# Kernel tuning notes

Measured on AMD Instinct MI355X. Metric: run time of the kernel, lower is better.

## Reference

```python
import jax, jax.numpy as jnp
import numpy as np

D_MODEL = 1024
NHEAD = 16
HEAD_DIM = D_MODEL // NHEAD


def setup_inputs() -> dict:
    key = jax.random.key(0)
    ks = jax.random.split(key, 11)
    B, T = 2, 2048
    s = 1.0 / np.sqrt(D_MODEL)
    return {
        "query": jax.random.normal(ks[0], (B, T, D_MODEL), jnp.float32),
        "key": jax.random.normal(ks[1], (B, T, D_MODEL), jnp.float32),
        "value": jax.random.normal(ks[2], (B, T, D_MODEL), jnp.float32),
        "Wq": jax.random.normal(ks[3], (D_MODEL, D_MODEL), jnp.float32) * s,
        "bq": jnp.zeros((D_MODEL,), jnp.float32),
        "Wk": jax.random.normal(ks[4], (D_MODEL, D_MODEL), jnp.float32) * s,
        "bk": jnp.zeros((D_MODEL,), jnp.float32),
        "Wv": jax.random.normal(ks[5], (D_MODEL, D_MODEL), jnp.float32) * s,
        "bv": jnp.zeros((D_MODEL,), jnp.float32),
        "Wo": jax.random.normal(ks[6], (D_MODEL, D_MODEL), jnp.float32) * s,
        "bo": jnp.zeros((D_MODEL,), jnp.float32),
    }


def reference(query, key, value, Wq, bq, Wk, bk, Wv, bv, Wo, bo):
    B, T, _ = query.shape
    scale = HEAD_DIM ** -0.5
    # Linear projections (torch Linear: x @ W.T + b)
    Q = query @ Wq.T + bq
    K = key @ Wk.T + bk
    V = value @ Wv.T + bv
    # [B, H, T, hd]
    Q = Q.reshape(B, T, NHEAD, HEAD_DIM).transpose(0, 2, 1, 3)
    K = K.reshape(B, T, NHEAD, HEAD_DIM).transpose(0, 2, 1, 3)
    V = V.reshape(B, T, NHEAD, HEAD_DIM).transpose(0, 2, 1, 3)
    # Attention scores [B, H, T, T]
    scores = jnp.einsum("bhqd,bhkd->bhqk", Q, K) * scale
    probs = jax.nn.softmax(scores, axis=-1)
    # dropout is identity in eval mode
    out = jnp.einsum("bhqk,bhkd->bhqd", probs, V)
    out = out.transpose(0, 2, 1, 3).reshape(B, T, D_MODEL)
    return out @ Wo.T + bo
```

## Files before the change

kernel.cpp:

```cpp
#include <hip/hip_runtime.h>
#include <stdint.h>

#define LOG2E_OVER_SQRTHD 0.18033688011112042f
#define SM_BIAS 12.0f

typedef unsigned short u16;
typedef _Float16 f16;
typedef __attribute__((ext_vector_type(4))) float f32x4;
typedef __attribute__((ext_vector_type(16))) float f32x16;
typedef __attribute__((ext_vector_type(8))) _Float16 f16x8;
typedef __attribute__((ext_vector_type(2))) __fp16 fp16x2;
typedef __attribute__((ext_vector_type(2))) unsigned int u32x2v;

static __device__ __forceinline__ u16 f2h_bits(float f) {
  union { f16 h; u16 u; } v; v.h = (f16)f; return v.u;
}
static __device__ __forceinline__ uint32_t pkrtz(float a, float b) {
  union { fp16x2 h; uint32_t u; } v;
  v.h = __builtin_amdgcn_cvt_pkrtz(a, b);
  return v.u;
}

static __device__ __forceinline__ void g2l16(const void* g, void* l) {
  __builtin_amdgcn_global_load_lds((const __attribute__((address_space(1))) void*)g,
                                   (__attribute__((address_space(3))) void*)l,
                                   16, 0, 0);
}

__global__ __launch_bounds__(256) void pack_all(
    const float* __restrict__ q, const float* __restrict__ k, const float* __restrict__ v,
    const float* __restrict__ wq, const float* __restrict__ wk,
    const float* __restrict__ wv, const float* __restrict__ wo,
    u16* __restrict__ X, u16* __restrict__ W) {
  int flat = blockIdx.x * 256 + threadIdx.x;
  const float* src;
  u16* dst;
  int idx;
  if (flat < 3 * 1048576) {
    int z = flat >> 20;
    idx = flat & 1048575;
    src = (z == 0) ? q : (z == 1) ? k : v;
    dst = X + (size_t)z * 4194304;
  } else {
    int f2 = flat - 3 * 1048576;
    int z = f2 >> 18;
    idx = f2 & 262143;
    src = (z == 0) ? wq : (z == 1) ? wk : (z == 2) ? wv : wo;
    dst = W + (size_t)z * 1048576;
  }
  float4 x = ((const float4*)src)[idx];
  ushort4 o;
  o.x = f2h_bits(x.x); o.y = f2h_bits(x.y); o.z = f2h_bits(x.z); o.w = f2h_bits(x.w);
  *(ushort4*)(dst + (size_t)idx * 4) = o;
}

template <bool OUT_F16>
static __device__ __forceinline__ void gemm_body(
    const u16* __restrict__ A, const u16* __restrict__ W,
    const float* __restrict__ bias, void* __restrict__ C,
    int ldc, bool row_bias, float oscale, int bm, int bn) {
  __shared__ u16 As[2][128 * 32];
  __shared__ u16 Bs[2][128 * 32];
  const int tid = threadIdx.x;
  const int lane = tid & 63;
  const int wave = tid >> 6;
  const int wm = wave >> 1, wn = wave & 1;
  const int quad = lane >> 4, l15 = lane & 15;

  f32x4 acc[4][4] = {};

  const int r0 = tid >> 2;
  const int c0 = (tid & 3) * 8;
  const u16* Ab = A + (size_t)bm * 1024 + (size_t)r0 * 1024 + c0;
  const u16* Wb = W + (size_t)bn * 1024 + (size_t)r0 * 1024 + c0;

  g2l16(Ab, As[0] + tid * 8);
  g2l16(Ab + 64 * 1024, As[0] + (256 + tid) * 8);
  g2l16(Wb, Bs[0] + tid * 8);
  g2l16(Wb + 64 * 1024, Bs[0] + (256 + tid) * 8);
  __syncthreads();

  for (int kt = 0; kt < 32; ++kt) {
    const int p = kt & 1;
    if (kt + 1 < 32) {
      const int kc = (kt + 1) * 32;
      g2l16(Ab + kc, As[p ^ 1] + tid * 8);
      g2l16(Ab + 64 * 1024 + kc, As[p ^ 1] + (256 + tid) * 8);
      g2l16(Wb + kc, Bs[p ^ 1] + tid * 8);
      g2l16(Wb + 64 * 1024 + kc, Bs[p ^ 1] + (256 + tid) * 8);
    }
    f16x8 af[4], bw[4];
#pragma unroll
    for (int mt = 0; mt < 4; ++mt)
      af[mt] = *(const f16x8*)(As[p] + (wm * 64 + mt * 16 + l15) * 32 + quad * 8);
#pragma unroll
    for (int nt = 0; nt < 4; ++nt)
      bw[nt] = *(const f16x8*)(Bs[p] + (wn * 64 + nt * 16 + l15) * 32 + quad * 8);
#pragma unroll
    for (int mt = 0; mt < 4; ++mt)
#pragma unroll
      for (int nt = 0; nt < 4; ++nt)
        acc[mt][nt] = __builtin_amdgcn_mfma_f32_16x16x32_f16(af[mt], bw[nt], acc[mt][nt], 0, 0, 0);
    __syncthreads();
  }

#pragma unroll
  for (int mt = 0; mt < 4; ++mt) {
    const int row = bm + wm * 64 + mt * 16 + quad * 4;
#pragma unroll
    for (int nt = 0; nt < 4; ++nt) {
      const int col = bn + wn * 64 + nt * 16 + l15;
      const float bcol = row_bias ? 0.0f : bias[col];
#pragma unroll
      for (int i = 0; i < 4; ++i) {
        const float bb = row_bias ? bias[row + i] : bcol;
        float val = (acc[mt][nt][i] + bb) * oscale;
        if (OUT_F16)
          ((u16*)C)[(size_t)(row + i) * ldc + col] = f2h_bits(val);
        else
          ((float*)C)[(size_t)(row + i) * ldc + col] = val;
      }
    }
  }
}

__global__ __launch_bounds__(256) void gemm_qkv(const u16* __restrict__ X,
    const u16* __restrict__ Wf, const float* __restrict__ bq,
    const float* __restrict__ bk, const float* __restrict__ bv,
    u16* __restrict__ QK, u16* __restrict__ Vt, float qscale) {
  const int i = blockIdx.x;
  const int xcd = i & 7;
  const int jj = i >> 3;
  const int x = jj & 31;
  const int pl = jj >> 5;
  const int pg = xcd + 8 * pl;
  const int y = pg & 7, z = pg >> 3;
  if (z == 0) {
    gemm_body<true>(X, Wf, bq, QK, 1024, false, qscale,
                    x * 128, y * 128);
  } else if (z == 1) {
    gemm_body<true>(X + (size_t)4194304, Wf + (size_t)1048576, bk,
                    QK + (size_t)4194304, 1024, false, 1.0f,
                    x * 128, y * 128);
  } else {
    gemm_body<true>(Wf + (size_t)2 * 1048576, X + (size_t)2 * 4194304, bv,
                    Vt, 4096, true, 1.0f,
                    y * 128, x * 128);
  }
}

__global__ __launch_bounds__(256) void gemm_out64(const u16* __restrict__ O,
    const u16* __restrict__ Wo, const float* __restrict__ bo,
    float* __restrict__ out) {
  __shared__ u16 As[2][64 * 64];
  __shared__ u16 Bs[2][64 * 64];
  const int tid = threadIdx.x;
  const int lane = tid & 63;
  const int wave = tid >> 6;
  const int wm = wave >> 1, wn = wave & 1;
  const int quad = lane >> 4, l15 = lane & 15;
  const int bm = blockIdx.x * 64, bn = blockIdx.y * 64;

  f32x4 acc[2][2] = {};

  const int rs = tid >> 3;
  const int cs = (tid & 7) * 8;
  const u16* Ab = O + (size_t)(bm + rs) * 1024 + cs;
  const u16* Wb = Wo + (size_t)(bn + rs) * 1024 + cs;

  g2l16(Ab, As[0] + tid * 8);
  g2l16(Ab + 32 * 1024, As[0] + (256 + tid) * 8);
  g2l16(Wb, Bs[0] + tid * 8);
  g2l16(Wb + 32 * 1024, Bs[0] + (256 + tid) * 8);
  __syncthreads();

  for (int kt = 0; kt < 16; ++kt) {
    const int p = kt & 1;
    if (kt + 1 < 16) {
      const int kc = (kt + 1) * 64;
      g2l16(Ab + kc, As[p ^ 1] + tid * 8);
      g2l16(Ab + 32 * 1024 + kc, As[p ^ 1] + (256 + tid) * 8);
      g2l16(Wb + kc, Bs[p ^ 1] + tid * 8);
      g2l16(Wb + 32 * 1024 + kc, Bs[p ^ 1] + (256 + tid) * 8);
    }
#pragma unroll
    for (int kk = 0; kk < 2; ++kk) {
      f16x8 af[2], bw[2];
#pragma unroll
      for (int mt = 0; mt < 2; ++mt)
        af[mt] = *(const f16x8*)(As[p] + (wm * 32 + mt * 16 + l15) * 64 + kk * 32 + quad * 8);
#pragma unroll
      for (int nt = 0; nt < 2; ++nt)
        bw[nt] = *(const f16x8*)(Bs[p] + (wn * 32 + nt * 16 + l15) * 64 + kk * 32 + quad * 8);
#pragma unroll
      for (int mt = 0; mt < 2; ++mt)
#pragma unroll
        for (int nt = 0; nt < 2; ++nt)
          acc[mt][nt] = __builtin_amdgcn_mfma_f32_16x16x32_f16(af[mt], bw[nt], acc[mt][nt], 0, 0, 0);
    }
    __syncthreads();
  }

#pragma unroll
  for (int mt = 0; mt < 2; ++mt) {
    const int row = bm + wm * 32 + mt * 16 + quad * 4;
#pragma unroll
    for (int nt = 0; nt < 2; ++nt) {
      const int col = bn + wn * 32 + nt * 16 + l15;
      const float bcol = bo[col];
#pragma unroll
      for (int i = 0; i < 4; ++i)
        out[(size_t)(row + i) * 1024 + col] = acc[mt][nt][i] + bcol;
    }
  }
}

__global__ __launch_bounds__(512, 4) void attn_kernel(const u16* __restrict__ QK,
                                                      const u16* __restrict__ Vt,
                                                      u16* __restrict__ O) {
  __shared__ u16 lds[40960];
  u16* Qs = lds;

  const u16* Qb = QK;
  const u16* Kb = QK + (size_t)4096 * 1024;

  const int tid = threadIdx.x, lane = tid & 63, wave = tid >> 6;
  const int q31 = lane & 31, hh = lane >> 5;
  const int set = wave >> 2, w4 = wave & 3;

  const int id = blockIdx.x;
  const int xcd = id & 7;
  const int j = id >> 3;
  const int qt = j & 15;
  const int hb = xcd + 8 * (j >> 4);
  const int h = hb & 15, b = hb >> 4;

  const size_t qrow0 = (size_t)b * 2048 + qt * 128;
  const size_t kv0 = (size_t)b * 2048;
  const int hc = h * 64;

  const int rq = tid >> 3;
  const int pq = tid & 7;
  const int sq = (pq ^ (rq & 7)) * 8;
  g2l16(Qb + (qrow0 + rq) * 1024 + hc + sq, Qs + tid * 8);
  g2l16(Qb + (qrow0 + 64 + rq) * 1024 + hc + sq, Qs + (512 + tid) * 8);

  const int st = tid & 255;
  const int r0 = st >> 3;
  const int p0 = st & 7;
  const int s0 = (p0 ^ (r0 & 7)) * 8;

  const int kt0 = set * 16;
  u16* KsS  = lds + 8192  + set * 8192;
  u16* VtsS = lds + 24576 + set * 8192;

  {
    const size_t kr = kv0 + (size_t)kt0 * 64;
    g2l16(Kb + (kr + r0) * 1024 + hc + s0, KsS + st * 8);
    g2l16(Kb + (kr + 32 + r0) * 1024 + hc + s0, KsS + (256 + st) * 8);
    g2l16(Vt + (size_t)(hc + r0) * 4096 + kr + s0, VtsS + st * 8);
    g2l16(Vt + (size_t)(hc + 32 + r0) * 4096 + kr + s0, VtsS + (256 + st) * 8);
  }
  __syncthreads();

  const size_t kr1_0 = kv0 + (size_t)(kt0 + 1) * 64;
  const u16* kpre0 = Kb + (kr1_0 + r0) * 1024 + hc + s0;
  const u16* kpre1 = Kb + (kr1_0 + 32 + r0) * 1024 + hc + s0;
  const u16* vpre0 = Vt + (size_t)(hc + r0) * 4096 + kr1_0 + s0;
  const u16* vpre1 = Vt + (size_t)(hc + 32 + r0) * 4096 + kr1_0 + s0;

  f16x8 qf[4];
  const int Rq = w4 * 32 + q31;
#pragma unroll
  for (int c = 0; c < 4; ++c)
    qf[c] = *(const f16x8*)(Qs + Rq * 64 + (((2 * c + hh) ^ (Rq & 7)) * 8));

  f32x16 oacc[2] = {};
  float l_lane = 0.f;

  for (int it = 0; it < 16; ++it) {
    const int p = it & 1;
    if (it + 1 < 16) {
      u16* Kd = KsS + (p ^ 1) * 4096;
      u16* Vd = VtsS + (p ^ 1) * 4096;
      g2l16(kpre0, Kd + st * 8);
      g2l16(kpre1, Kd + (256 + st) * 8);
      g2l16(vpre0, Vd + st * 8);
      g2l16(vpre1, Vd + (256 + st) * 8);
      kpre0 += 64 * 1024; kpre1 += 64 * 1024;
      vpre0 += 64;        vpre1 += 64;
    }
    const u16* Kc = KsS + p * 4096;
    const u16* Vc = VtsS + p * 4096;

    f32x16 sac[2];
#pragma unroll
    for (int t = 0; t < 2; ++t)
#pragma unroll
      for (int r = 0; r < 16; ++r) sac[t][r] = -SM_BIAS;
    __builtin_amdgcn_s_setprio(1);
#pragma unroll
    for (int t = 0; t < 2; ++t) {
      const int Rk = t * 32 + q31;
#pragma unroll
      for (int c = 0; c < 4; ++c) {
        f16x8 kf = *(const f16x8*)(Kc + Rk * 64 + (((2 * c + hh) ^ (Rk & 7)) * 8));
        sac[t] = __builtin_amdgcn_mfma_f32_32x32x16_f16(kf, qf[c], sac[t], 0, 0, 0);
      }
    }
    __builtin_amdgcn_s_setprio(0);

    uint32_t dd[2][8];
#pragma unroll
    for (int t = 0; t < 2; ++t) {
      float pe[16];
#pragma unroll
      for (int r = 0; r < 16; ++r) pe[r] = __builtin_amdgcn_exp2f(sac[t][r]);
      float a0 = (pe[0] + pe[1]) + (pe[2] + pe[3]);
      float a1 = (pe[4] + pe[5]) + (pe[6] + pe[7]);
      float a2 = (pe[8] + pe[9]) + (pe[10] + pe[11]);
      float a3 = (pe[12] + pe[13]) + (pe[14] + pe[15]);
      l_lane += (a0 + a1) + (a2 + a3);
#pragma unroll
      for (int k = 0; k < 8; ++k) dd[t][k] = pkrtz(pe[2 * k], pe[2 * k + 1]);
    }

    f16x8 pf[4];
#pragma unroll
    for (int t = 0; t < 2; ++t) {
      u32x2v s02 = __builtin_amdgcn_permlane32_swap(dd[t][0], dd[t][2], 0, 0);
      u32x2v s13 = __builtin_amdgcn_permlane32_swap(dd[t][1], dd[t][3], 0, 0);
      u32x2v s46 = __builtin_amdgcn_permlane32_swap(dd[t][4], dd[t][6], 0, 0);
      u32x2v s57 = __builtin_amdgcn_permlane32_swap(dd[t][5], dd[t][7], 0, 0);
      union { uint32_t w[4]; f16x8 v; } f0, f1;
      f0.w[0] = s02[0]; f0.w[1] = s13[0]; f0.w[2] = s02[1]; f0.w[3] = s13[1];
      f1.w[0] = s46[0]; f1.w[1] = s57[0]; f1.w[2] = s46[1]; f1.w[3] = s57[1];
      pf[2 * t]     = f0.v;
      pf[2 * t + 1] = f1.v;
    }

    __builtin_amdgcn_s_setprio(1);
#pragma unroll
    for (int dt2 = 0; dt2 < 2; ++dt2) {
      const int Rv = dt2 * 32 + q31;
#pragma unroll
      for (int ch = 0; ch < 4; ++ch) {
        f16x8 vf = *(const f16x8*)(Vc + Rv * 64 + (((2 * ch + hh) ^ (Rv & 7)) * 8));
        oacc[dt2] = __builtin_amdgcn_mfma_f32_32x32x16_f16(vf, pf[ch], oacc[dt2], 0, 0, 0);
      }
    }
    __builtin_amdgcn_s_setprio(0);

    __syncthreads();
  }

  const float l_set = l_lane + __shfl_xor(l_lane, 32);

  float* Of = (float*)(lds + 24576);
  float* Ll = (float*)lds;
  u16* bounce = lds + 8192;
  const int orow = w4 * 32 + q31;

  if (set == 1) {
#pragma unroll
    for (int dt2 = 0; dt2 < 2; ++dt2)
#pragma unroll
      for (int r = 0; r < 16; ++r) {
        const int d = dt2 * 32 + (r & 3) + 8 * (r >> 2) + 4 * hh;
        Of[d * 128 + orow] = oacc[dt2][r];
      }
    if (hh == 0) Ll[orow] = l_set;
  }
  __syncthreads();

  if (set == 0) {
    const float inv = 1.0f / (l_set + Ll[orow]);
#pragma unroll
    for (int dt2 = 0; dt2 < 2; ++dt2)
#pragma unroll
      for (int w = 0; w < 8; ++w) {
        const int dbase = dt2 * 32 + 4 * hh + 8 * (w >> 1) + 2 * (w & 1);
        float va = (oacc[dt2][2 * w]     + Of[dbase * 128 + orow]) * inv;
        float vb = (oacc[dt2][2 * w + 1] + Of[(dbase + 1) * 128 + orow]) * inv;
        uint32_t pk2 = (uint32_t)f2h_bits(va) | ((uint32_t)f2h_bits(vb) << 16);
        *(uint32_t*)(bounce + orow * 72 + dbase) = pk2;
      }
  }
  __syncthreads();

  const int row2 = tid >> 2, q2 = tid & 3;
#pragma unroll
  for (int k = 0; k < 2; ++k) {
    const int chunk = q2 + 4 * k;
    uint4 v4 = *(const uint4*)(bounce + row2 * 72 + chunk * 8);
    *(uint4*)(O + (qrow0 + row2) * 1024 + hc + chunk * 8) = v4;
  }
}

extern "C" void kernel_launch(void* const* d_in, const int* in_sizes, int n_in,
                              void* d_out, int out_size, void* d_ws, size_t ws_size,
                              hipStream_t stream) {
  const float* query = (const float*)d_in[0];
  const float* key   = (const float*)d_in[1];
  const float* value = (const float*)d_in[2];
  const float* Wq = (const float*)d_in[3];
  const float* bq = (const float*)d_in[4];
  const float* Wk = (const float*)d_in[5];
  const float* bk = (const float*)d_in[6];
  const float* Wv = (const float*)d_in[7];
  const float* bv = (const float*)d_in[8];
  const float* Wo = (const float*)d_in[9];
  const float* bo = (const float*)d_in[10];
  float* out = (float*)d_out;

  u16* X  = (u16*)d_ws;
  u16* W  = X + (size_t)3 * 4194304;
  u16* QK = W + (size_t)4 * 1048576;
  u16* Vt = QK + (size_t)2 * 4194304;
  u16* O  = X;

  pack_all<<<dim3(16384, 1, 1), 256, 0, stream>>>(query, key, value, Wq, Wk, Wv, Wo, X, W);
  gemm_qkv<<<dim3(768, 1, 1), 256, 0, stream>>>(X, W, bq, bk, bv, QK, Vt,
                                                LOG2E_OVER_SQRTHD);
  attn_kernel<<<dim3(512, 1, 1), 512, 0, stream>>>(QK, Vt, O);
  gemm_out64<<<dim3(64, 16, 1), 256, 0, stream>>>(O, W + (size_t)3 * 1048576, bo, out);
}
```

Before: 221.0 us.

## Fuse fp32-to-fp16 activation conversion into QKV GEMM loads

The separate pass that converted query/key/value to fp16 is removed. The QKV GEMM now loads fp32 activations directly into registers, converts them to fp16 with round-to-nearest-even and writes them to LDS after the MFMA step, which overlaps the conversion with compute. Only the weights are still pre-packed. This avoids writing and re-reading the fp16 activation copy, but each GEMM tile now reads twice the bytes per element and uses register-staged loads instead of direct global-to-LDS transfers. The grid also drops the XCD-aware block remapping for a plain 3D grid, which may hurt L2 locality.

```diff
diff --git a/kernel.cpp b/kernel.cpp
--- a/kernel.cpp
+++ b/kernel.cpp
@@ -20,6 +20,14 @@
   v.h = __builtin_amdgcn_cvt_pkrtz(a, b);
   return v.u;
 }
+static __device__ __forceinline__ uint4 cvt8rne(float4 a, float4 b) {
+  uint4 r;
+  r.x = (uint32_t)f2h_bits(a.x) | ((uint32_t)f2h_bits(a.y) << 16);
+  r.y = (uint32_t)f2h_bits(a.z) | ((uint32_t)f2h_bits(a.w) << 16);
+  r.z = (uint32_t)f2h_bits(b.x) | ((uint32_t)f2h_bits(b.y) << 16);
+  r.w = (uint32_t)f2h_bits(b.z) | ((uint32_t)f2h_bits(b.w) << 16);
+  return r;
+}
 
 static __device__ __forceinline__ void g2l16(const void* g, void* l) {
   __builtin_amdgcn_global_load_lds((const __attribute__((address_space(1))) void*)g,
@@ -27,36 +35,24 @@
                                    16, 0, 0);
 }
 
-__global__ __launch_bounds__(256) void pack_all(
-    const float* __restrict__ q, const float* __restrict__ k, const float* __restrict__ v,
+__global__ __launch_bounds__(256) void pack_w(
     const float* __restrict__ wq, const float* __restrict__ wk,
     const float* __restrict__ wv, const float* __restrict__ wo,
-    u16* __restrict__ X, u16* __restrict__ W) {
+    u16* __restrict__ W) {
   int flat = blockIdx.x * 256 + threadIdx.x;
-  const float* src;
-  u16* dst;
-  int idx;
-  if (flat < 3 * 1048576) {
-    int z = flat >> 20;
-    idx = flat & 1048575;
-    src = (z == 0) ? q : (z == 1) ? k : v;
-    dst = X + (size_t)z * 4194304;
-  } else {
-    int f2 = flat - 3 * 1048576;
-    int z = f2 >> 18;
-    idx = f2 & 262143;
-    src = (z == 0) ? wq : (z == 1) ? wk : (z == 2) ? wv : wo;
-    dst = W + (size_t)z * 1048576;
-  }
+  int z = flat >> 18;
+  int idx = flat & 262143;
+  const float* src = (z == 0) ? wq : (z == 1) ? wk : (z == 2) ? wv : wo;
+  u16* dst = W + (size_t)z * 1048576;
   float4 x = ((const float4*)src)[idx];
   ushort4 o;
   o.x = f2h_bits(x.x); o.y = f2h_bits(x.y); o.z = f2h_bits(x.z); o.w = f2h_bits(x.w);
   *(ushort4*)(dst + (size_t)idx * 4) = o;
 }
 
-template <bool OUT_F16>
+template <bool OUT_F16, int CVT>
 static __device__ __forceinline__ void gemm_body(
-    const u16* __restrict__ A, const u16* __restrict__ W,
+    const void* __restrict__ Ap, const void* __restrict__ Bp,
     const float* __restrict__ bias, void* __restrict__ C,
     int ldc, bool row_bias, float oscale, int bm, int bn) {
   __shared__ u16 As[2][128 * 32];
@@ -71,23 +67,59 @@
 
   const int r0 = tid >> 2;
   const int c0 = (tid & 3) * 8;
-  const u16* Ab = A + (size_t)bm * 1024 + (size_t)r0 * 1024 + c0;
-  const u16* Wb = W + (size_t)bn * 1024 + (size_t)r0 * 1024 + c0;
-
-  g2l16(Ab, As[0] + tid * 8);
-  g2l16(Ab + 64 * 1024, As[0] + (256 + tid) * 8);
-  g2l16(Wb, Bs[0] + tid * 8);
-  g2l16(Wb + 64 * 1024, Bs[0] + (256 + tid) * 8);
+  const u16*   Ah = (const u16*)Ap   + (size_t)(bm + r0) * 1024 + c0;
+  const float* Af = (const float*)Ap + (size_t)(bm + r0) * 1024 + c0;
+  const u16*   Bh = (const u16*)Bp   + (size_t)(bn + r0) * 1024 + c0;
+  const float* Bf = (const float*)Bp + (size_t)(bn + r0) * 1024 + c0;
+
+  if (CVT == 1) {
+    float4 a0 = *(const float4*)(Af);
+    float4 a1 = *(const float4*)(Af + 4);
+    float4 a2 = *(const float4*)(Af + (size_t)64 * 1024);
+    float4 a3 = *(const float4*)(Af + (size_t)64 * 1024 + 4);
+    *(uint4*)(As[0] + tid * 8) = cvt8rne(a0, a1);
+    *(uint4*)(As[0] + (256 + tid) * 8) = cvt8rne(a2, a3);
+  } else {
+    g2l16(Ah, As[0] + tid * 8);
+    g2l16(Ah + 64 * 1024, As[0] + (256 + tid) * 8);
+  }
+  if (CVT == 2) {
+    float4 b0 = *(const float4*)(Bf);
+    float4 b1 = *(const float4*)(Bf + 4);
+    float4 b2 = *(const float4*)(Bf + (size_t)64 * 1024);
+    float4 b3 = *(const float4*)(Bf + (size_t)64 * 1024 + 4);
+    *(uint4*)(Bs[0] + tid * 8) = cvt8rne(b0, b1);
+    *(uint4*)(Bs[0] + (256 + tid) * 8) = cvt8rne(b2, b3);
+  } else {
+    g2l16(Bh, Bs[0] + tid * 8);
+    g2l16(Bh + 64 * 1024, Bs[0] + (256 + tid) * 8);
+  }
   __syncthreads();
 
   for (int kt = 0; kt < 32; ++kt) {
     const int p = kt & 1;
-    if (kt + 1 < 32) {
+    const bool pre = (kt + 1 < 32);
+    float4 pa0, pa1, pa2, pa3;
+    if (pre) {
       const int kc = (kt + 1) * 32;
-      g2l16(Ab + kc, As[p ^ 1] + tid * 8);
-      g2l16(Ab + 64 * 1024 + kc, As[p ^ 1] + (256 + tid) * 8);
-      g2l16(Wb + kc, Bs[p ^ 1] + tid * 8);
-      g2l16(Wb + 64 * 1024 + kc, Bs[p ^ 1] + (256 + tid) * 8);
+      if (CVT == 1) {
+        pa0 = *(const float4*)(Af + kc);
+        pa1 = *(const float4*)(Af + kc + 4);
+        pa2 = *(const float4*)(Af + (size_t)64 * 1024 + kc);
+        pa3 = *(const float4*)(Af + (size_t)64 * 1024 + kc + 4);
+      } else {
+        g2l16(Ah + kc, As[p ^ 1] + tid * 8);
+        g2l16(Ah + 64 * 1024 + kc, As[p ^ 1] + (256 + tid) * 8);
+      }
+      if (CVT == 2) {
+        pa0 = *(const float4*)(Bf + kc);
+        pa1 = *(const float4*)(Bf + kc + 4);
+        pa2 = *(const float4*)(Bf + (size_t)64 * 1024 + kc);
+        pa3 = *(const float4*)(Bf + (size_t)64 * 1024 + kc + 4);
+      } else {
+        g2l16(Bh + kc, Bs[p ^ 1] + tid * 8);
+        g2l16(Bh + 64 * 1024 + kc, Bs[p ^ 1] + (256 + tid) * 8);
+      }
     }
     f16x8 af[4], bw[4];
 #pragma unroll
@@ -101,6 +133,11 @@
 #pragma unroll
       for (int nt = 0; nt < 4; ++nt)
         acc[mt][nt] = __builtin_amdgcn_mfma_f32_16x16x32_f16(af[mt], bw[nt], acc[mt][nt], 0, 0, 0);
+    if (pre && CVT != 0) {
+      u16* dst = (CVT == 1) ? As[p ^ 1] : Bs[p ^ 1];
+      *(uint4*)(dst + tid * 8) = cvt8rne(pa0, pa1);
+      *(uint4*)(dst + (256 + tid) * 8) = cvt8rne(pa2, pa3);
+    }
     __syncthreads();
   }
 
@@ -124,28 +161,24 @@
   }
 }
 
-__global__ __launch_bounds__(256) void gemm_qkv(const u16* __restrict__ X,
-    const u16* __restrict__ Wf, const float* __restrict__ bq,
-    const float* __restrict__ bk, const float* __restrict__ bv,
-    u16* __restrict__ QK, u16* __restrict__ Vt, float qscale) {
-  const int i = blockIdx.x;
-  const int xcd = i & 7;
-  const int jj = i >> 3;
-  const int x = jj & 31;
-  const int pl = jj >> 5;
-  const int pg = xcd + 8 * pl;
-  const int y = pg & 7, z = pg >> 3;
+__global__ __launch_bounds__(256) void gemm_qkv(
+    const float* __restrict__ query, const float* __restrict__ key,
+    const float* __restrict__ value, const u16* __restrict__ Wf,
+    const float* __restrict__ bq, const float* __restrict__ bk,
+    const float* __restrict__ bv, u16* __restrict__ QK,
+    u16* __restrict__ Vt, float qscale) {
+  const int z = blockIdx.z;
   if (z == 0) {
-    gemm_body<true>(X, Wf, bq, QK, 1024, false, qscale,
-                    x * 128, y * 128);
+    gemm_body<true, 1>(query, Wf, bq, QK, 1024, false, qscale,
+                       blockIdx.x * 128, blockIdx.y * 128);
   } else if (z == 1) {
-    gemm_body<true>(X + (size_t)4194304, Wf + (size_t)1048576, bk,
-                    QK + (size_t)4194304, 1024, false, 1.0f,
-                    x * 128, y * 128);
+    gemm_body<true, 1>(key, Wf + (size_t)1048576, bk,
+                       QK + (size_t)4194304, 1024, false, 1.0f,
+                       blockIdx.x * 128, blockIdx.y * 128);
   } else {
-    gemm_body<true>(Wf + (size_t)2 * 1048576, X + (size_t)2 * 4194304, bv,
-                    Vt, 4096, true, 1.0f,
-                    y * 128, x * 128);
+    gemm_body<true, 2>(Wf + (size_t)2 * 1048576, value, bv,
+                       Vt, 4096, true, 1.0f,
+                       blockIdx.y * 128, blockIdx.x * 128);
   }
 }
 
@@ -419,9 +452,10 @@
   u16* Vt = QK + (size_t)2 * 4194304;
   u16* O  = X;
 
-  pack_all<<<dim3(16384, 1, 1), 256, 0, stream>>>(query, key, value, Wq, Wk, Wv, Wo, X, W);
-  gemm_qkv<<<dim3(768, 1, 1), 256, 0, stream>>>(X, W, bq, bk, bv, QK, Vt,
-                                                LOG2E_OVER_SQRTHD);
+  pack_w<<<dim3(4096, 1, 1), 256, 0, stream>>>(Wq, Wk, Wv, Wo, W);
+  gemm_qkv<<<dim3(32, 8, 3), 256, 0, stream>>>(query, key, value, W,
+                                               bq, bk, bv, QK, Vt,
+                                               LOG2E_OVER_SQRTHD);
   attn_kernel<<<dim3(512, 1, 1), 512, 0, stream>>>(QK, Vt, O);
   gemm_out64<<<dim3(64, 16, 1), 256, 0, stream>>>(O, W + (size_t)3 * 1048576, bo, out);
 }
```

Result: slower. 267.3 us (+20.9%).
